# Optimization experiments

Measured on AMD Instinct MI355X. Metric: run time of the kernel, lower is better.

Reference implementation:

```python
import jax, jax.numpy as jnp
import numpy as np

# ---- grid / spectral configuration (matches init_kwargs) ----
_LONS_HALF = [20 + 4 * i for i in range(1, 97)]
LONS = _LONS_HALF + _LONS_HALF[::-1]          # 192 rings, pole to pole
NLAT = len(LONS)                               # 192
TRUNC = 191
M = TRUNC + 1                                  # zonal wavenumbers kept
MAX_NLON = max(LONS)                           # 404
SLON = np.concatenate([[0], np.cumsum(LONS)[:-1]]).astype(np.int64)
NGRID = int(np.sum(LONS))                      # 41088
BATCH, CHAN = 16, 64
TWO_PI = 2.0 * np.pi


def _legpoly(mmax, lmax, x):
    """(-1)^m c^l_m P^l_m(x), shape (mmax+1, lmax+1, len(x)); same recurrences as source."""
    nmax = max(mmax, lmax)
    vdm = np.zeros((nmax + 1, nmax + 1, len(x)), dtype=np.float64)
    norm_factor = np.sqrt(4 * np.pi)  # forward transform (inverse=False)
    vdm[0, 0, :] = norm_factor / np.sqrt(4 * np.pi)
    for n in range(1, nmax + 1):
        vdm[n - 1, n, :] = np.sqrt(2 * n + 1) * x * vdm[n - 1, n - 1, :]
        vdm[n, n, :] = np.sqrt((2 * n + 1) * (1 + x) * (1 - x) / 2 / n) * vdm[n - 1, n - 1, :]
    for n in range(2, nmax + 1):
        for m in range(0, n - 1):
            vdm[m, n, :] = (x * np.sqrt((2 * n - 1) / (n - m) * (2 * n + 1) / (n + m)) * vdm[m, n - 1, :]
                            - np.sqrt((n + m - 1) / (n - m) * (2 * n + 1) / (2 * n - 3) * (n - m - 1) / (n + m)) * vdm[m, n - 2, :])
    return vdm[:mmax + 1, :lmax + 1]


def _build_buffers():
    # Legendre-Gauss nodes/weights on [-1, 1]
    xlg, wlg = np.polynomial.legendre.leggauss(NLAT)
    theta = np.flip(np.arccos(xlg))
    pct = _legpoly(TRUNC, TRUNC, np.cos(theta))          # (M, L, K)
    weight = (pct * wlg[None, None, :]).astype(np.float32)

    # Ragged per-ring real DFT expressed as masked cos/sin bases (== rfft, norm='forward')
    p = np.arange(MAX_NLON)
    m = np.arange(M)
    nlon = np.asarray(LONS, dtype=np.float64)[:, None, None]       # (K,1,1)
    ang = TWO_PI * m[None, None, :] * p[None, :, None] / nlon      # (K,P,M)
    valid = (p[None, :, None] < nlon) & (m[None, None, :] <= (np.asarray(LONS)[:, None, None] // 2))
    cos_basis = np.where(valid, np.cos(ang) / nlon, 0.0).astype(np.float32)
    sin_basis = np.where(valid, -np.sin(ang) / nlon, 0.0).astype(np.float32)

    # gather map: ring_idx[k, p] = SLON[k] + min(p, nlon_k - 1)  (clipped; basis masks the tail)
    ring_idx = (SLON[:, None] + np.minimum(p[None, :], np.asarray(LONS)[:, None] - 1)).astype(np.int32)
    return weight, cos_basis, sin_basis, ring_idx


def setup_inputs() -> dict:
    key = jax.random.key(0)
    x = jax.random.normal(key, (BATCH, CHAN, NGRID), dtype=jnp.float32)
    weight, cos_basis, sin_basis, ring_idx = _build_buffers()
    return {
        "x": x,
        "weight": jnp.asarray(weight),
        "cos_basis": jnp.asarray(cos_basis),
        "sin_basis": jnp.asarray(sin_basis),
        "ring_idx": jnp.asarray(ring_idx),
    }


def reference(x, weight, cos_basis, sin_basis, ring_idx):
    # gather grid points into padded rings: [..., K, P]
    xr = x[..., ring_idx]
    # per-ring rfft (norm='forward'), restricted to m <= TRUNC, scaled by 2*pi
    re = TWO_PI * jnp.einsum("bckp,kpm->bckm", xr, cos_basis)
    im = TWO_PI * jnp.einsum("bckp,kpm->bckm", xr, sin_basis)
    # weighted Legendre contraction over latitudes k: [..., l, m]
    rl = jnp.einsum("bckm,mlk->bclm", re, weight)
    il = jnp.einsum("bckm,mlk->bclm", im, weight)
    # real/imag stacked (== torch.view_as_real of the complex output)
    return jnp.stack((rl, il), axis=-1)
```

## Files before the change

### kernel.cpp

```cpp
#include <hip/hip_runtime.h>

#define NLAT 192
#define MM   192
#define LL   192
#define PMAX 404
#define NGRID 41088
#define BC   1024
#define TWO_PI_F 6.2831853071795864769f

__global__ __launch_bounds__(256) void sht_stage1(
    const float* __restrict__ x,
    const float* __restrict__ cosb,
    const float* __restrict__ sinb,
    const int*   __restrict__ ring,
    float* __restrict__ ws,
    int bc0, int bcc)
{
    const int k   = blockIdx.z;
    const int m0  = blockIdx.y * 64;
    const int bct = blockIdx.x * 64;
    const int tid = threadIdx.x;
    const int tx = tid & 15;
    const int ty = tid >> 4;

    const int slon = ring[k * PMAX];
    const int nlon = ring[k * PMAX + PMAX - 1] - slon + 1;

    float* __restrict__ re_ws = ws;
    float* __restrict__ im_ws = ws + (size_t)MM * NLAT * bcc;

    if (m0 > (nlon >> 1)) {
        float4 z = {0.f, 0.f, 0.f, 0.f};
#pragma unroll
        for (int j = 0; j < 4; ++j) {
            int m = m0 + 4 * ty + j;
            size_t base = ((size_t)m * NLAT + k) * bcc + bct + 4 * tx;
            *(float4*)&re_ws[base] = z;
            *(float4*)&im_ws[base] = z;
        }
        return;
    }

    __shared__ float xs[16][68];
    __shared__ float cs[16][64];
    __shared__ float ss[16][64];

    float accr[4][4] = {{0.f}};
    float acci[4][4] = {{0.f}};

    for (int p0 = 0; p0 < nlon; p0 += 16) {
        {
            int pq = (tid & 3) * 4;
            int bl = tid >> 2;
            int p  = p0 + pq;
            float4 v = {0.f, 0.f, 0.f, 0.f};
            if (p < nlon)
                v = *(const float4*)(x + (size_t)(bc0 + bct + bl) * NGRID + slon + p);
            xs[pq + 0][bl] = v.x;
            xs[pq + 1][bl] = v.y;
            xs[pq + 2][bl] = v.z;
            xs[pq + 3][bl] = v.w;
        }
        {
            int mq = (tid & 15) * 4;
            int pl = tid >> 4;
            int p  = p0 + pl;
            float4 c = {0.f, 0.f, 0.f, 0.f};
            float4 s = {0.f, 0.f, 0.f, 0.f};
            if (p < PMAX) {
                size_t off = ((size_t)k * PMAX + p) * MM + m0 + mq;
                c = *(const float4*)(cosb + off);
                s = *(const float4*)(sinb + off);
            }
            *(float4*)&cs[pl][mq] = c;
            *(float4*)&ss[pl][mq] = s;
        }
        __syncthreads();

#pragma unroll
        for (int pp = 0; pp < 16; ++pp) {
            float xv[4], cv[4], sv[4];
            *(float4*)xv = *(const float4*)&xs[pp][4 * tx];
            *(float4*)cv = *(const float4*)&cs[pp][4 * ty];
            *(float4*)sv = *(const float4*)&ss[pp][4 * ty];
#pragma unroll
            for (int i = 0; i < 4; ++i)
#pragma unroll
                for (int j = 0; j < 4; ++j) {
                    accr[i][j] += xv[i] * cv[j];
                    acci[i][j] += xv[i] * sv[j];
                }
        }
        __syncthreads();
    }

#pragma unroll
    for (int j = 0; j < 4; ++j) {
        int m = m0 + 4 * ty + j;
        size_t base = ((size_t)m * NLAT + k) * bcc + bct + 4 * tx;
        float4 r = {accr[0][j] * TWO_PI_F, accr[1][j] * TWO_PI_F,
                    accr[2][j] * TWO_PI_F, accr[3][j] * TWO_PI_F};
        float4 s = {acci[0][j] * TWO_PI_F, acci[1][j] * TWO_PI_F,
                    acci[2][j] * TWO_PI_F, acci[3][j] * TWO_PI_F};
        *(float4*)&re_ws[base] = r;
        *(float4*)&im_ws[base] = s;
    }
}

__global__ __launch_bounds__(256) void sht_stage2(
    const float* __restrict__ ws,
    float* __restrict__ ws2,
    const float* __restrict__ weight,
    int bcc)
{
    const int m   = blockIdx.z;
    const int l0  = blockIdx.y * 64;
    const int bct = blockIdx.x * 64;
    const int tid = threadIdx.x;
    const int tx = tid & 15;
    const int ty = tid >> 4;

    if (l0 + 63 < m) return;

    const float* __restrict__ re_ws = ws;
    const float* __restrict__ im_ws = ws + (size_t)MM * NLAT * bcc;

    __shared__ float rs[16][64];
    __shared__ float is_[16][64];
    __shared__ float wl[16][68];

    float accr[4][4] = {{0.f}};
    float acci[4][4] = {{0.f}};

    for (int k0 = 0; k0 < NLAT; k0 += 16) {
        {
            int bl = tid & 63;
            int kk = tid >> 6;
#pragma unroll
            for (int kp = 0; kp < 4; ++kp) {
                int row = kk + kp * 4;
                size_t off = ((size_t)m * NLAT + k0 + row) * bcc + bct + bl;
                rs[row][bl]  = re_ws[off];
                is_[row][bl] = im_ws[off];
            }
        }
        {
            int kk = tid & 15;
            int ll = tid >> 4;
#pragma unroll
            for (int lp = 0; lp < 4; ++lp) {
                int l = l0 + ll + lp * 16;
                wl[kk][ll + lp * 16] = weight[((size_t)m * LL + l) * NLAT + k0 + kk];
            }
        }
        __syncthreads();

#pragma unroll
        for (int kk = 0; kk < 16; ++kk) {
            float rv[4], iv[4], wv[4];
            *(float4*)rv = *(const float4*)&rs[kk][4 * tx];
            *(float4*)iv = *(const float4*)&is_[kk][4 * tx];
            *(float4*)wv = *(const float4*)&wl[kk][4 * ty];
#pragma unroll
            for (int i = 0; i < 4; ++i)
#pragma unroll
                for (int j = 0; j < 4; ++j) {
                    accr[i][j] += rv[i] * wv[j];
                    acci[i][j] += iv[i] * wv[j];
                }
        }
        __syncthreads();
    }

    float* __restrict__ re2 = ws2;
    float* __restrict__ im2 = ws2 + (size_t)MM * LL * bcc;
#pragma unroll
    for (int j = 0; j < 4; ++j) {
        int l = l0 + 4 * ty + j;
        size_t base = ((size_t)m * LL + l) * bcc + bct + 4 * tx;
        float4 r = {accr[0][j], accr[1][j], accr[2][j], accr[3][j]};
        float4 s = {acci[0][j], acci[1][j], acci[2][j], acci[3][j]};
        *(float4*)&re2[base] = r;
        *(float4*)&im2[base] = s;
    }
}

__global__ __launch_bounds__(256) void sht_transpose(
    const float* __restrict__ ws2,
    float* __restrict__ out,
    int bc0, int bcc)
{
    const int l   = blockIdx.z;
    const int m0  = blockIdx.y * 32;
    const int bct = blockIdx.x * 32;
    const int tid = threadIdx.x;

    const float* __restrict__ re2 = ws2;
    const float* __restrict__ im2 = ws2 + (size_t)MM * LL * bcc;

    __shared__ float tr[32][33];
    __shared__ float ti[32][33];

    if (m0 <= l) {
        int bci = tid & 31;
        int mi  = tid >> 5;
#pragma unroll
        for (int mp = 0; mp < 4; ++mp) {
            int mrow = mi + mp * 8;
            size_t off = ((size_t)(m0 + mrow) * LL + l) * bcc + bct + bci;
            tr[mrow][bci] = re2[off];
            ti[mrow][bci] = im2[off];
        }
    }
    __syncthreads();

    int mi2  = tid & 31;
    int bci2 = tid >> 5;
    int m = m0 + mi2;
    bool nz = (m <= l);
#pragma unroll
    for (int bcp = 0; bcp < 4; ++bcp) {
        int bcl = bci2 + bcp * 8;
        int bc  = bc0 + bct + bcl;
        float2 v;
        if (nz) { v.x = tr[mi2][bcl]; v.y = ti[mi2][bcl]; }
        else    { v.x = 0.f;          v.y = 0.f;          }
        size_t o = (((size_t)bc * LL + l) * MM + m) * 2;
        *(float2*)&out[o] = v;
    }
}

extern "C" void kernel_launch(void* const* d_in, const int* in_sizes, int n_in,
                              void* d_out, int out_size, void* d_ws, size_t ws_size,
                              hipStream_t stream)
{
    const float* x      = (const float*)d_in[0];
    const float* weight = (const float*)d_in[1];
    const float* cosb   = (const float*)d_in[2];
    const float* sinb   = (const float*)d_in[3];
    const int*   ring   = (const int*)d_in[4];
    float* out = (float*)d_out;
    float* wsf = (float*)d_ws;

    const size_t per_bc = 4ull * MM * NLAT * sizeof(float);
    int chunk = BC;
    while ((size_t)chunk * per_bc > ws_size && chunk > 64) chunk >>= 1;

    for (int bc0 = 0; bc0 < BC; bc0 += chunk) {
        float* ws2 = wsf + 2ull * MM * NLAT * chunk;
        dim3 grid1(chunk / 64, 3, NLAT);
        hipLaunchKernelGGL(sht_stage1, grid1, dim3(256), 0, stream,
                           x, cosb, sinb, ring, wsf, bc0, chunk);
        dim3 grid2(chunk / 64, 3, MM);
        hipLaunchKernelGGL(sht_stage2, grid2, dim3(256), 0, stream,
                           wsf, ws2, weight, chunk);
        dim3 grid3(chunk / 32, 6, LL);
        hipLaunchKernelGGL(sht_transpose, grid3, dim3(256), 0, stream,
                           ws2, out, bc0, chunk);
    }
}
```

Measured before the change: 1.025 ms.

## Widen batch tiles and skip latitudes where Legendre weights vanish

Doubles the batch-channel tile in the DFT and Legendre stages to 128, so each thread computes an 8x4 register tile and reuses the shared basis and weights across more batch columns. Stage 2 now starts and ends its latitude loop at a polar cutoff kmin_of_m(m), skipping rows where the associated Legendre weights are assumed negligible. Stage 1 stops writing zeros for those skipped rows, and the transpose moves to 64x64 tiles with float4 loads and stores. The tile change raises register pressure and halves the block count. The latitude cutoff drops terms that are small but not exactly zero, so results may deviate slightly.

Measured after the change: 972.5 us. -5.1%, faster.

```diff
diff --git a/kernel.cpp b/kernel.cpp
--- a/kernel.cpp
+++ b/kernel.cpp
@@ -8,6 +8,10 @@
 #define BC   1024
 #define TWO_PI_F 6.2831853071795864769f
 
+__device__ __forceinline__ int kmin_of_m(int m) {
+    return (m <= 12) ? 0 : ((m - 11) >> 1);
+}
+
 __global__ __launch_bounds__(256) void sht_stage1(
     const float* __restrict__ x,
     const float* __restrict__ cosb,
@@ -18,10 +22,10 @@
 {
     const int k   = blockIdx.z;
     const int m0  = blockIdx.y * 64;
-    const int bct = blockIdx.x * 64;
+    const int bct = blockIdx.x * 128;
     const int tid = threadIdx.x;
-    const int tx = tid & 15;
-    const int ty = tid >> 4;
+    const int tx  = tid & 15;
+    const int ty  = tid >> 4;
 
     const int slon = ring[k * PMAX];
     const int nlon = ring[k * PMAX + PMAX - 1] - slon + 1;
@@ -30,45 +34,48 @@
     float* __restrict__ im_ws = ws + (size_t)MM * NLAT * bcc;
 
     if (m0 > (nlon >> 1)) {
-        float4 z = {0.f, 0.f, 0.f, 0.f};
+        const int klo16 = kmin_of_m(m0) & ~15;
+        if (k < klo16 || k > (NLAT - 1) - klo16) return;
+        const float4 z = {0.f, 0.f, 0.f, 0.f};
 #pragma unroll
         for (int j = 0; j < 4; ++j) {
-            int m = m0 + 4 * ty + j;
-            size_t base = ((size_t)m * NLAT + k) * bcc + bct + 4 * tx;
-            *(float4*)&re_ws[base] = z;
-            *(float4*)&im_ws[base] = z;
+            const int m = m0 + 4 * ty + j;
+            const size_t base = ((size_t)m * NLAT + k) * bcc + bct;
+            *(float4*)&re_ws[base + 4 * tx]      = z;
+            *(float4*)&re_ws[base + 64 + 4 * tx] = z;
+            *(float4*)&im_ws[base + 4 * tx]      = z;
+            *(float4*)&im_ws[base + 64 + 4 * tx] = z;
         }
         return;
     }
 
-    __shared__ float xs[16][68];
+    __shared__ float xs[16][128];
     __shared__ float cs[16][64];
     __shared__ float ss[16][64];
 
-    float accr[4][4] = {{0.f}};
-    float acci[4][4] = {{0.f}};
+    float accr[8][4] = {{0.f}};
+    float acci[8][4] = {{0.f}};
 
     for (int p0 = 0; p0 < nlon; p0 += 16) {
-        {
-            int pq = (tid & 3) * 4;
-            int bl = tid >> 2;
-            int p  = p0 + pq;
+#pragma unroll
+        for (int r = 0; r < 2; ++r) {
+            const int idx = r * 256 + tid;
+            const int bl  = idx & 127;
+            const int pq  = (idx >> 7) * 4;
             float4 v = {0.f, 0.f, 0.f, 0.f};
-            if (p < nlon)
-                v = *(const float4*)(x + (size_t)(bc0 + bct + bl) * NGRID + slon + p);
+            if (p0 + pq < nlon)
+                v = *(const float4*)(x + (size_t)(bc0 + bct + bl) * NGRID + slon + p0 + pq);
             xs[pq + 0][bl] = v.x;
             xs[pq + 1][bl] = v.y;
             xs[pq + 2][bl] = v.z;
             xs[pq + 3][bl] = v.w;
         }
         {
-            int mq = (tid & 15) * 4;
-            int pl = tid >> 4;
-            int p  = p0 + pl;
-            float4 c = {0.f, 0.f, 0.f, 0.f};
-            float4 s = {0.f, 0.f, 0.f, 0.f};
-            if (p < PMAX) {
-                size_t off = ((size_t)k * PMAX + p) * MM + m0 + mq;
+            const int mq = tx * 4;
+            const int pl = ty;
+            float4 c = {0.f, 0.f, 0.f, 0.f}, s = {0.f, 0.f, 0.f, 0.f};
+            if (p0 + pl < PMAX) {
+                const size_t off = ((size_t)k * PMAX + p0 + pl) * MM + m0 + mq;
                 c = *(const float4*)(cosb + off);
                 s = *(const float4*)(sinb + off);
             }
@@ -79,16 +86,19 @@
 
 #pragma unroll
         for (int pp = 0; pp < 16; ++pp) {
-            float xv[4], cv[4], sv[4];
-            *(float4*)xv = *(const float4*)&xs[pp][4 * tx];
-            *(float4*)cv = *(const float4*)&cs[pp][4 * ty];
-            *(float4*)sv = *(const float4*)&ss[pp][4 * ty];
-#pragma unroll
-            for (int i = 0; i < 4; ++i)
+            const float4 xa = *(const float4*)&xs[pp][4 * tx];
+            const float4 xb = *(const float4*)&xs[pp][64 + 4 * tx];
+            const float4 cv = *(const float4*)&cs[pp][4 * ty];
+            const float4 sv = *(const float4*)&ss[pp][4 * ty];
+            const float xv[8] = {xa.x, xa.y, xa.z, xa.w, xb.x, xb.y, xb.z, xb.w};
+            const float cw[4] = {cv.x, cv.y, cv.z, cv.w};
+            const float sw[4] = {sv.x, sv.y, sv.z, sv.w};
+#pragma unroll
+            for (int i = 0; i < 8; ++i)
 #pragma unroll
                 for (int j = 0; j < 4; ++j) {
-                    accr[i][j] += xv[i] * cv[j];
-                    acci[i][j] += xv[i] * sv[j];
+                    accr[i][j] += xv[i] * cw[j];
+                    acci[i][j] += xv[i] * sw[j];
                 }
         }
         __syncthreads();
@@ -96,14 +106,20 @@
 
 #pragma unroll
     for (int j = 0; j < 4; ++j) {
-        int m = m0 + 4 * ty + j;
-        size_t base = ((size_t)m * NLAT + k) * bcc + bct + 4 * tx;
-        float4 r = {accr[0][j] * TWO_PI_F, accr[1][j] * TWO_PI_F,
-                    accr[2][j] * TWO_PI_F, accr[3][j] * TWO_PI_F};
-        float4 s = {acci[0][j] * TWO_PI_F, acci[1][j] * TWO_PI_F,
-                    acci[2][j] * TWO_PI_F, acci[3][j] * TWO_PI_F};
-        *(float4*)&re_ws[base] = r;
-        *(float4*)&im_ws[base] = s;
+        const int m = m0 + 4 * ty + j;
+        const size_t base = ((size_t)m * NLAT + k) * bcc + bct;
+        float4 r0 = {accr[0][j] * TWO_PI_F, accr[1][j] * TWO_PI_F,
+                     accr[2][j] * TWO_PI_F, accr[3][j] * TWO_PI_F};
+        float4 r1 = {accr[4][j] * TWO_PI_F, accr[5][j] * TWO_PI_F,
+                     accr[6][j] * TWO_PI_F, accr[7][j] * TWO_PI_F};
+        float4 i0 = {acci[0][j] * TWO_PI_F, acci[1][j] * TWO_PI_F,
+                     acci[2][j] * TWO_PI_F, acci[3][j] * TWO_PI_F};
+        float4 i1 = {acci[4][j] * TWO_PI_F, acci[5][j] * TWO_PI_F,
+                     acci[6][j] * TWO_PI_F, acci[7][j] * TWO_PI_F};
+        *(float4*)&re_ws[base + 4 * tx]      = r0;
+        *(float4*)&re_ws[base + 64 + 4 * tx] = r1;
+        *(float4*)&im_ws[base + 4 * tx]      = i0;
+        *(float4*)&im_ws[base + 64 + 4 * tx] = i1;
     }
 }
 
@@ -115,58 +131,66 @@
 {
     const int m   = blockIdx.z;
     const int l0  = blockIdx.y * 64;
-    const int bct = blockIdx.x * 64;
+    const int bct = blockIdx.x * 128;
     const int tid = threadIdx.x;
-    const int tx = tid & 15;
-    const int ty = tid >> 4;
+    const int tx  = tid & 15;
+    const int ty  = tid >> 4;
 
     if (l0 + 63 < m) return;
+
+    const int klo16 = kmin_of_m(m) & ~15;
+    const int kcnt  = NLAT - 2 * klo16;
 
     const float* __restrict__ re_ws = ws;
     const float* __restrict__ im_ws = ws + (size_t)MM * NLAT * bcc;
 
-    __shared__ float rs[16][64];
-    __shared__ float is_[16][64];
-    __shared__ float wl[16][68];
-
-    float accr[4][4] = {{0.f}};
-    float acci[4][4] = {{0.f}};
-
-    for (int k0 = 0; k0 < NLAT; k0 += 16) {
+    __shared__ float rs[16][128];
+    __shared__ float is_[16][128];
+    __shared__ float wl[16][64];
+
+    float accr[8][4] = {{0.f}};
+    float acci[8][4] = {{0.f}};
+
+    for (int kc = 0; kc < kcnt; kc += 16) {
+        const int k0 = klo16 + kc;
         {
-            int bl = tid & 63;
-            int kk = tid >> 6;
-#pragma unroll
-            for (int kp = 0; kp < 4; ++kp) {
-                int row = kk + kp * 4;
-                size_t off = ((size_t)m * NLAT + k0 + row) * bcc + bct + bl;
-                rs[row][bl]  = re_ws[off];
-                is_[row][bl] = im_ws[off];
+            const int bl4 = (tid & 31) * 4;
+            const int kk  = tid >> 5;
+#pragma unroll
+            for (int r = 0; r < 2; ++r) {
+                const int row = kk + r * 8;
+                const size_t off = ((size_t)m * NLAT + k0 + row) * bcc + bct + bl4;
+                *(float4*)&rs[row][bl4]  = *(const float4*)&re_ws[off];
+                *(float4*)&is_[row][bl4] = *(const float4*)&im_ws[off];
             }
         }
         {
-            int kk = tid & 15;
-            int ll = tid >> 4;
-#pragma unroll
-            for (int lp = 0; lp < 4; ++lp) {
-                int l = l0 + ll + lp * 16;
-                wl[kk][ll + lp * 16] = weight[((size_t)m * LL + l) * NLAT + k0 + kk];
+            const int kk = tid & 15;
+            const int lw = tid >> 4;
+#pragma unroll
+            for (int r = 0; r < 4; ++r) {
+                const int lc = lw + r * 16;
+                wl[kk][lc] = weight[((size_t)m * LL + l0 + lc) * NLAT + k0 + kk];
             }
         }
         __syncthreads();
 
 #pragma unroll
         for (int kk = 0; kk < 16; ++kk) {
-            float rv[4], iv[4], wv[4];
-            *(float4*)rv = *(const float4*)&rs[kk][4 * tx];
-            *(float4*)iv = *(const float4*)&is_[kk][4 * tx];
-            *(float4*)wv = *(const float4*)&wl[kk][4 * ty];
-#pragma unroll
-            for (int i = 0; i < 4; ++i)
+            const float4 ra = *(const float4*)&rs[kk][4 * tx];
+            const float4 rb = *(const float4*)&rs[kk][64 + 4 * tx];
+            const float4 ia = *(const float4*)&is_[kk][4 * tx];
+            const float4 ib = *(const float4*)&is_[kk][64 + 4 * tx];
+            const float4 wv = *(const float4*)&wl[kk][4 * ty];
+            const float rv[8] = {ra.x, ra.y, ra.z, ra.w, rb.x, rb.y, rb.z, rb.w};
+            const float iv[8] = {ia.x, ia.y, ia.z, ia.w, ib.x, ib.y, ib.z, ib.w};
+            const float wq[4] = {wv.x, wv.y, wv.z, wv.w};
+#pragma unroll
+            for (int i = 0; i < 8; ++i)
 #pragma unroll
                 for (int j = 0; j < 4; ++j) {
-                    accr[i][j] += rv[i] * wv[j];
-                    acci[i][j] += iv[i] * wv[j];
+                    accr[i][j] += rv[i] * wq[j];
+                    acci[i][j] += iv[i] * wq[j];
                 }
         }
         __syncthreads();
@@ -176,12 +200,17 @@
     float* __restrict__ im2 = ws2 + (size_t)MM * LL * bcc;
 #pragma unroll
     for (int j = 0; j < 4; ++j) {
-        int l = l0 + 4 * ty + j;
-        size_t base = ((size_t)m * LL + l) * bcc + bct + 4 * tx;
-        float4 r = {accr[0][j], accr[1][j], accr[2][j], accr[3][j]};
-        float4 s = {acci[0][j], acci[1][j], acci[2][j], acci[3][j]};
-        *(float4*)&re2[base] = r;
-        *(float4*)&im2[base] = s;
+        const int l = l0 + 4 * ty + j;
+        if (l < m) continue;
+        const size_t base = ((size_t)m * LL + l) * bcc + bct;
+        float4 r0 = {accr[0][j], accr[1][j], accr[2][j], accr[3][j]};
+        float4 r1 = {accr[4][j], accr[5][j], accr[6][j], accr[7][j]};
+        float4 i0 = {acci[0][j], acci[1][j], acci[2][j], acci[3][j]};
+        float4 i1 = {acci[4][j], acci[5][j], acci[6][j], acci[7][j]};
+        *(float4*)&re2[base + 4 * tx]      = r0;
+        *(float4*)&re2[base + 64 + 4 * tx] = r1;
+        *(float4*)&im2[base + 4 * tx]      = i0;
+        *(float4*)&im2[base + 64 + 4 * tx] = i1;
     }
 }
 
@@ -191,42 +220,47 @@
     int bc0, int bcc)
 {
     const int l   = blockIdx.z;
-    const int m0  = blockIdx.y * 32;
-    const int bct = blockIdx.x * 32;
+    const int m0  = blockIdx.y * 64;
+    const int bct = blockIdx.x * 64;
     const int tid = threadIdx.x;
 
-    const float* __restrict__ re2 = ws2;
-    const float* __restrict__ im2 = ws2 + (size_t)MM * LL * bcc;
-
-    __shared__ float tr[32][33];
-    __shared__ float ti[32][33];
-
-    if (m0 <= l) {
-        int bci = tid & 31;
-        int mi  = tid >> 5;
-#pragma unroll
-        for (int mp = 0; mp < 4; ++mp) {
-            int mrow = mi + mp * 8;
-            size_t off = ((size_t)(m0 + mrow) * LL + l) * bcc + bct + bci;
-            tr[mrow][bci] = re2[off];
-            ti[mrow][bci] = im2[off];
+    __shared__ float tr[64][66];
+    __shared__ float ti[64][66];
+
+    const bool anynz = (m0 <= l);
+    if (anynz) {
+        const float* __restrict__ re2 = ws2;
+        const float* __restrict__ im2 = ws2 + (size_t)MM * LL * bcc;
+        const int bl4 = (tid & 15) * 4;
+        const int mr  = tid >> 4;
+#pragma unroll
+        for (int r = 0; r < 4; ++r) {
+            const int row = mr + r * 16;
+            const size_t off = ((size_t)(m0 + row) * LL + l) * bcc + bct + bl4;
+            *(float4*)&tr[row][bl4] = *(const float4*)&re2[off];
+            *(float4*)&ti[row][bl4] = *(const float4*)&im2[off];
         }
     }
     __syncthreads();
 
-    int mi2  = tid & 31;
-    int bci2 = tid >> 5;
-    int m = m0 + mi2;
-    bool nz = (m <= l);
-#pragma unroll
-    for (int bcp = 0; bcp < 4; ++bcp) {
-        int bcl = bci2 + bcp * 8;
-        int bc  = bc0 + bct + bcl;
-        float2 v;
-        if (nz) { v.x = tr[mi2][bcl]; v.y = ti[mi2][bcl]; }
-        else    { v.x = 0.f;          v.y = 0.f;          }
-        size_t o = (((size_t)bc * LL + l) * MM + m) * 2;
-        *(float2*)&out[o] = v;
+    const int mq  = tid & 15;
+    const int bcw = tid >> 4;
+#pragma unroll
+    for (int r = 0; r < 4; ++r) {
+        const int bcl = bcw + r * 16;
+        const int bc  = bc0 + bct + bcl;
+#pragma unroll
+        for (int h = 0; h < 2; ++h) {
+            const int ml = 32 * h + 2 * mq;
+            const int m  = m0 + ml;
+            float4 v = {0.f, 0.f, 0.f, 0.f};
+            if (anynz) {
+                if (m <= l)     { v.x = tr[ml][bcl];     v.y = ti[ml][bcl]; }
+                if (m + 1 <= l) { v.z = tr[ml + 1][bcl]; v.w = ti[ml + 1][bcl]; }
+            }
+            const size_t o = (((size_t)bc * LL + l) * MM + m) * 2;
+            *(float4*)&out[o] = v;
+        }
     }
 }
 
@@ -244,17 +278,17 @@
 
     const size_t per_bc = 4ull * MM * NLAT * sizeof(float);
     int chunk = BC;
-    while ((size_t)chunk * per_bc > ws_size && chunk > 64) chunk >>= 1;
+    while ((size_t)chunk * per_bc > ws_size && chunk > 128) chunk >>= 1;
 
     for (int bc0 = 0; bc0 < BC; bc0 += chunk) {
         float* ws2 = wsf + 2ull * MM * NLAT * chunk;
-        dim3 grid1(chunk / 64, 3, NLAT);
+        dim3 grid1(chunk / 128, 3, NLAT);
         hipLaunchKernelGGL(sht_stage1, grid1, dim3(256), 0, stream,
                            x, cosb, sinb, ring, wsf, bc0, chunk);
-        dim3 grid2(chunk / 64, 3, MM);
+        dim3 grid2(chunk / 128, 3, MM);
         hipLaunchKernelGGL(sht_stage2, grid2, dim3(256), 0, stream,
                            wsf, ws2, weight, chunk);
-        dim3 grid3(chunk / 32, 6, LL);
+        dim3 grid3(chunk / 64, 3, LL);
         hipLaunchKernelGGL(sht_transpose, grid3, dim3(256), 0, stream,
                            ws2, out, bc0, chunk);
     }
```

## Exploit Legendre even/odd symmetry and skip negligible latitudes in the SHT stages

Applied to the files above, without the earlier changes.

Stage 2 folds north/south rings into even and odd sums and contracts only half the latitudes, picking the even or odd combination per l parity. It also skips latitude tiles below a per-m cutoff where the Legendre weights are negligible, and skips writes for l < m. Stage 1 doubles the batch tile to 128 with 512-thread blocks and skips zero-fills outside the needed latitude range. The transpose kernel is widened to 64 m per block and writes float4. The latitude cutoff is an approximation that relies on small weights, so it risks accuracy. Fewer, larger blocks may also hurt occupancy.

Result: slower. 1.940 ms (+89.2%).

```diff
diff --git a/kernel.cpp b/kernel.cpp
--- a/kernel.cpp
+++ b/kernel.cpp
@@ -8,7 +8,11 @@
 #define BC   1024
 #define TWO_PI_F 6.2831853071795864769f
 
-__global__ __launch_bounds__(256) void sht_stage1(
+__device__ __forceinline__ int kmin_of_m(int m) {
+    return (m <= 12) ? 0 : ((m - 11) >> 1);
+}
+
+__global__ __launch_bounds__(512, 8) void sht_stage1(
     const float* __restrict__ x,
     const float* __restrict__ cosb,
     const float* __restrict__ sinb,
@@ -18,10 +22,10 @@
 {
     const int k   = blockIdx.z;
     const int m0  = blockIdx.y * 64;
-    const int bct = blockIdx.x * 64;
+    const int bct = blockIdx.x * 128;
     const int tid = threadIdx.x;
-    const int tx = tid & 15;
-    const int ty = tid >> 4;
+    const int tx  = tid & 31;
+    const int ty  = (tid >> 5) & 15;
 
     const int slon = ring[k * PMAX];
     const int nlon = ring[k * PMAX + PMAX - 1] - slon + 1;
@@ -30,65 +34,67 @@
     float* __restrict__ im_ws = ws + (size_t)MM * NLAT * bcc;
 
     if (m0 > (nlon >> 1)) {
-        float4 z = {0.f, 0.f, 0.f, 0.f};
+        const int klo16 = kmin_of_m(m0) & ~15;
+        if (k < klo16 || k > (NLAT - 1) - klo16) return;
+        const float4 z = {0.f, 0.f, 0.f, 0.f};
 #pragma unroll
         for (int j = 0; j < 4; ++j) {
-            int m = m0 + 4 * ty + j;
-            size_t base = ((size_t)m * NLAT + k) * bcc + bct + 4 * tx;
+            const int m = m0 + 4 * ty + j;
+            const size_t base = ((size_t)m * NLAT + k) * bcc + bct + 4 * tx;
             *(float4*)&re_ws[base] = z;
             *(float4*)&im_ws[base] = z;
         }
         return;
     }
 
-    __shared__ float xs[16][68];
+    __shared__ float xs[16][128];
     __shared__ float cs[16][64];
     __shared__ float ss[16][64];
 
     float accr[4][4] = {{0.f}};
     float acci[4][4] = {{0.f}};
 
+    const int xpq  = (tid & 3) * 4;
+    const int xbl  = tid >> 2;
+    const int bpl  = (tid >> 4) & 15;
+    const int bmq  = (tid & 15) * 4;
+    const int half = tid >> 8;
+
     for (int p0 = 0; p0 < nlon; p0 += 16) {
         {
-            int pq = (tid & 3) * 4;
-            int bl = tid >> 2;
-            int p  = p0 + pq;
             float4 v = {0.f, 0.f, 0.f, 0.f};
-            if (p < nlon)
-                v = *(const float4*)(x + (size_t)(bc0 + bct + bl) * NGRID + slon + p);
-            xs[pq + 0][bl] = v.x;
-            xs[pq + 1][bl] = v.y;
-            xs[pq + 2][bl] = v.z;
-            xs[pq + 3][bl] = v.w;
-        }
-        {
-            int mq = (tid & 15) * 4;
-            int pl = tid >> 4;
-            int p  = p0 + pl;
-            float4 c = {0.f, 0.f, 0.f, 0.f};
-            float4 s = {0.f, 0.f, 0.f, 0.f};
-            if (p < PMAX) {
-                size_t off = ((size_t)k * PMAX + p) * MM + m0 + mq;
-                c = *(const float4*)(cosb + off);
-                s = *(const float4*)(sinb + off);
+            if (p0 + xpq < nlon)
+                v = *(const float4*)(x + (size_t)(bc0 + bct + xbl) * NGRID + slon + p0 + xpq);
+            xs[xpq + 0][xbl] = v.x;
+            xs[xpq + 1][xbl] = v.y;
+            xs[xpq + 2][xbl] = v.z;
+            xs[xpq + 3][xbl] = v.w;
+        }
+        {
+            float4 b = {0.f, 0.f, 0.f, 0.f};
+            if (p0 + bpl < PMAX) {
+                const size_t off = ((size_t)k * PMAX + p0 + bpl) * MM + m0 + bmq;
+                b = *(const float4*)((half ? sinb : cosb) + off);
             }
-            *(float4*)&cs[pl][mq] = c;
-            *(float4*)&ss[pl][mq] = s;
+            if (half) *(float4*)&ss[bpl][bmq] = b;
+            else      *(float4*)&cs[bpl][bmq] = b;
         }
         __syncthreads();
 
 #pragma unroll
         for (int pp = 0; pp < 16; ++pp) {
-            float xv[4], cv[4], sv[4];
-            *(float4*)xv = *(const float4*)&xs[pp][4 * tx];
-            *(float4*)cv = *(const float4*)&cs[pp][4 * ty];
-            *(float4*)sv = *(const float4*)&ss[pp][4 * ty];
+            const float4 xa = *(const float4*)&xs[pp][4 * tx];
+            const float4 cv = *(const float4*)&cs[pp][4 * ty];
+            const float4 sv = *(const float4*)&ss[pp][4 * ty];
+            const float xv[4] = {xa.x, xa.y, xa.z, xa.w};
+            const float cw[4] = {cv.x, cv.y, cv.z, cv.w};
+            const float sw[4] = {sv.x, sv.y, sv.z, sv.w};
 #pragma unroll
             for (int i = 0; i < 4; ++i)
 #pragma unroll
                 for (int j = 0; j < 4; ++j) {
-                    accr[i][j] += xv[i] * cv[j];
-                    acci[i][j] += xv[i] * sv[j];
+                    accr[i][j] += xv[i] * cw[j];
+                    acci[i][j] += xv[i] * sw[j];
                 }
         }
         __syncthreads();
@@ -96,8 +102,8 @@
 
 #pragma unroll
     for (int j = 0; j < 4; ++j) {
-        int m = m0 + 4 * ty + j;
-        size_t base = ((size_t)m * NLAT + k) * bcc + bct + 4 * tx;
+        const int m = m0 + 4 * ty + j;
+        const size_t base = ((size_t)m * NLAT + k) * bcc + bct + 4 * tx;
         float4 r = {accr[0][j] * TWO_PI_F, accr[1][j] * TWO_PI_F,
                     accr[2][j] * TWO_PI_F, accr[3][j] * TWO_PI_F};
         float4 s = {acci[0][j] * TWO_PI_F, acci[1][j] * TWO_PI_F,
@@ -107,7 +113,7 @@
     }
 }
 
-__global__ __launch_bounds__(256) void sht_stage2(
+__global__ __launch_bounds__(512, 8) void sht_stage2(
     const float* __restrict__ ws,
     float* __restrict__ ws2,
     const float* __restrict__ weight,
@@ -115,59 +121,81 @@
 {
     const int m   = blockIdx.z;
     const int l0  = blockIdx.y * 64;
-    const int bct = blockIdx.x * 64;
+    const int bct = blockIdx.x * 128;
+    if (l0 + 63 < m) return;
+
     const int tid = threadIdx.x;
-    const int tx = tid & 15;
-    const int ty = tid >> 4;
-
-    if (l0 + 63 < m) return;
+    const int tx  = tid & 31;
+    const int ty  = (tid >> 5) & 15;
+
+    const int klo16 = kmin_of_m(m) & ~15;
+    const int pcnt  = 96 - klo16;
 
     const float* __restrict__ re_ws = ws;
     const float* __restrict__ im_ws = ws + (size_t)MM * NLAT * bcc;
 
-    __shared__ float rs[16][64];
-    __shared__ float is_[16][64];
+    __shared__ float Ar[16][128];
+    __shared__ float Br[16][128];
+    __shared__ float Ai[16][128];
+    __shared__ float Bi[16][128];
     __shared__ float wl[16][68];
 
     float accr[4][4] = {{0.f}};
     float acci[4][4] = {{0.f}};
 
-    for (int k0 = 0; k0 < NLAT; k0 += 16) {
-        {
-            int bl = tid & 63;
-            int kk = tid >> 6;
-#pragma unroll
-            for (int kp = 0; kp < 4; ++kp) {
-                int row = kk + kp * 4;
-                size_t off = ((size_t)m * NLAT + k0 + row) * bcc + bct + bl;
-                rs[row][bl]  = re_ws[off];
-                is_[row][bl] = im_ws[off];
+    const bool modd = (m & 1) != 0;
+    const int  srow = tid >> 5;
+    const int  scol = (tid & 31) * 4;
+    const int  wkk  = tid & 15;
+    const int  wlw  = tid >> 4;
+
+    for (int pc = 0; pc < pcnt; pc += 16) {
+        const int p0 = klo16 + pc;
+        {
+            const size_t offa = ((size_t)m * NLAT + (p0 + srow)) * bcc + bct + scol;
+            const size_t offb = ((size_t)m * NLAT + (191 - p0 - srow)) * bcc + bct + scol;
+            const float4 ar = *(const float4*)&re_ws[offa];
+            const float4 br = *(const float4*)&re_ws[offb];
+            const float4 ai = *(const float4*)&im_ws[offa];
+            const float4 bi = *(const float4*)&im_ws[offb];
+            float4 er = {ar.x + br.x, ar.y + br.y, ar.z + br.z, ar.w + br.w};
+            float4 od = {ar.x - br.x, ar.y - br.y, ar.z - br.z, ar.w - br.w};
+            float4 ei = {ai.x + bi.x, ai.y + bi.y, ai.z + bi.z, ai.w + bi.w};
+            float4 oi = {ai.x - bi.x, ai.y - bi.y, ai.z - bi.z, ai.w - bi.w};
+            if (modd) { float4 t = er; er = od; od = t; t = ei; ei = oi; oi = t; }
+            *(float4*)&Ar[srow][scol] = er;
+            *(float4*)&Br[srow][scol] = od;
+            *(float4*)&Ai[srow][scol] = ei;
+            *(float4*)&Bi[srow][scol] = oi;
+        }
+        {
+            wl[wkk][wlw]      = weight[((size_t)m * LL + l0 + wlw) * NLAT + p0 + wkk];
+            wl[wkk][wlw + 32] = weight[((size_t)m * LL + l0 + wlw + 32) * NLAT + p0 + wkk];
+        }
+        __syncthreads();
+
+#pragma unroll
+        for (int kk = 0; kk < 16; ++kk) {
+            const float4 e_r = *(const float4*)&Ar[kk][4 * tx];
+            const float4 o_r = *(const float4*)&Br[kk][4 * tx];
+            const float4 e_i = *(const float4*)&Ai[kk][4 * tx];
+            const float4 o_i = *(const float4*)&Bi[kk][4 * tx];
+            const float4 wv  = *(const float4*)&wl[kk][4 * ty];
+            const float er4[4] = {e_r.x, e_r.y, e_r.z, e_r.w};
+            const float or4[4] = {o_r.x, o_r.y, o_r.z, o_r.w};
+            const float ei4[4] = {e_i.x, e_i.y, e_i.z, e_i.w};
+            const float oi4[4] = {o_i.x, o_i.y, o_i.z, o_i.w};
+#pragma unroll
+            for (int i = 0; i < 4; ++i) {
+                accr[i][0] += er4[i] * wv.x;
+                accr[i][1] += or4[i] * wv.y;
+                accr[i][2] += er4[i] * wv.z;
+                accr[i][3] += or4[i] * wv.w;
+                acci[i][0] += ei4[i] * wv.x;
+                acci[i][1] += oi4[i] * wv.y;
+                acci[i][2] += ei4[i] * wv.z;
+                acci[i][3] += oi4[i] * wv.w;
             }
-        }
-        {
-            int kk = tid & 15;
-            int ll = tid >> 4;
-#pragma unroll
-            for (int lp = 0; lp < 4; ++lp) {
-                int l = l0 + ll + lp * 16;
-                wl[kk][ll + lp * 16] = weight[((size_t)m * LL + l) * NLAT + k0 + kk];
-            }
-        }
-        __syncthreads();
-
-#pragma unroll
-        for (int kk = 0; kk < 16; ++kk) {
-            float rv[4], iv[4], wv[4];
-            *(float4*)rv = *(const float4*)&rs[kk][4 * tx];
-            *(float4*)iv = *(const float4*)&is_[kk][4 * tx];
-            *(float4*)wv = *(const float4*)&wl[kk][4 * ty];
-#pragma unroll
-            for (int i = 0; i < 4; ++i)
-#pragma unroll
-                for (int j = 0; j < 4; ++j) {
-                    accr[i][j] += rv[i] * wv[j];
-                    acci[i][j] += iv[i] * wv[j];
-                }
         }
         __syncthreads();
     }
@@ -176,8 +204,9 @@
     float* __restrict__ im2 = ws2 + (size_t)MM * LL * bcc;
 #pragma unroll
     for (int j = 0; j < 4; ++j) {
-        int l = l0 + 4 * ty + j;
-        size_t base = ((size_t)m * LL + l) * bcc + bct + 4 * tx;
+        const int l = l0 + 4 * ty + j;
+        if (l < m) continue;
+        const size_t base = ((size_t)m * LL + l) * bcc + bct + 4 * tx;
         float4 r = {accr[0][j], accr[1][j], accr[2][j], accr[3][j]};
         float4 s = {acci[0][j], acci[1][j], acci[2][j], acci[3][j]};
         *(float4*)&re2[base] = r;
@@ -191,42 +220,49 @@
     int bc0, int bcc)
 {
     const int l   = blockIdx.z;
-    const int m0  = blockIdx.y * 32;
+    const int m0  = blockIdx.y * 64;
     const int bct = blockIdx.x * 32;
     const int tid = threadIdx.x;
 
-    const float* __restrict__ re2 = ws2;
-    const float* __restrict__ im2 = ws2 + (size_t)MM * LL * bcc;
-
-    __shared__ float tr[32][33];
-    __shared__ float ti[32][33];
-
-    if (m0 <= l) {
-        int bci = tid & 31;
-        int mi  = tid >> 5;
-#pragma unroll
-        for (int mp = 0; mp < 4; ++mp) {
-            int mrow = mi + mp * 8;
-            size_t off = ((size_t)(m0 + mrow) * LL + l) * bcc + bct + bci;
-            tr[mrow][bci] = re2[off];
-            ti[mrow][bci] = im2[off];
+    __shared__ float t2r[32][66];
+    __shared__ float t2i[32][66];
+
+    const bool anynz = (m0 <= l);
+    if (anynz) {
+        const float* __restrict__ re2 = ws2;
+        const float* __restrict__ im2 = ws2 + (size_t)MM * LL * bcc;
+        const int bl4 = (tid & 7) * 4;
+        const int mr  = tid >> 3;
+#pragma unroll
+        for (int r = 0; r < 2; ++r) {
+            const int row = mr + r * 32;
+            const size_t off = ((size_t)(m0 + row) * LL + l) * bcc + bct + bl4;
+            const float4 a = *(const float4*)&re2[off];
+            const float4 b = *(const float4*)&im2[off];
+            t2r[bl4 + 0][row] = a.x; t2r[bl4 + 1][row] = a.y;
+            t2r[bl4 + 2][row] = a.z; t2r[bl4 + 3][row] = a.w;
+            t2i[bl4 + 0][row] = b.x; t2i[bl4 + 1][row] = b.y;
+            t2i[bl4 + 2][row] = b.z; t2i[bl4 + 3][row] = b.w;
         }
     }
     __syncthreads();
 
-    int mi2  = tid & 31;
-    int bci2 = tid >> 5;
-    int m = m0 + mi2;
-    bool nz = (m <= l);
-#pragma unroll
-    for (int bcp = 0; bcp < 4; ++bcp) {
-        int bcl = bci2 + bcp * 8;
-        int bc  = bc0 + bct + bcl;
-        float2 v;
-        if (nz) { v.x = tr[mi2][bcl]; v.y = ti[mi2][bcl]; }
-        else    { v.x = 0.f;          v.y = 0.f;          }
-        size_t o = (((size_t)bc * LL + l) * MM + m) * 2;
-        *(float2*)&out[o] = v;
+    const int mq  = tid & 31;
+    const int bcw = tid >> 5;
+#pragma unroll
+    for (int r = 0; r < 4; ++r) {
+        const int bcl = bcw + 8 * r;
+        const int bc  = bc0 + bct + bcl;
+        const int m   = m0 + 2 * mq;
+        float4 v = {0.f, 0.f, 0.f, 0.f};
+        if (anynz) {
+            const float2 rr = *(const float2*)&t2r[bcl][2 * mq];
+            const float2 ii = *(const float2*)&t2i[bcl][2 * mq];
+            if (m     <= l) { v.x = rr.x; v.y = ii.x; }
+            if (m + 1 <= l) { v.z = rr.y; v.w = ii.y; }
+        }
+        const size_t o = (((size_t)bc * LL + l) * MM + m) * 2;
+        *(float4*)&out[o] = v;
     }
 }
 
@@ -244,17 +280,17 @@
 
     const size_t per_bc = 4ull * MM * NLAT * sizeof(float);
     int chunk = BC;
-    while ((size_t)chunk * per_bc > ws_size && chunk > 64) chunk >>= 1;
+    while ((size_t)chunk * per_bc > ws_size && chunk > 128) chunk >>= 1;
 
     for (int bc0 = 0; bc0 < BC; bc0 += chunk) {
         float* ws2 = wsf + 2ull * MM * NLAT * chunk;
-        dim3 grid1(chunk / 64, 3, NLAT);
-        hipLaunchKernelGGL(sht_stage1, grid1, dim3(256), 0, stream,
+        dim3 grid1(chunk / 128, 3, NLAT);
+        hipLaunchKernelGGL(sht_stage1, grid1, dim3(512), 0, stream,
                            x, cosb, sinb, ring, wsf, bc0, chunk);
-        dim3 grid2(chunk / 64, 3, MM);
-        hipLaunchKernelGGL(sht_stage2, grid2, dim3(256), 0, stream,
+        dim3 grid2(chunk / 128, 3, MM);
+        hipLaunchKernelGGL(sht_stage2, grid2, dim3(512), 0, stream,
                            wsf, ws2, weight, chunk);
-        dim3 grid3(chunk / 32, 6, LL);
+        dim3 grid3(chunk / 32, 3, LL);
         hipLaunchKernelGGL(sht_transpose, grid3, dim3(256), 0, stream,
                            ws2, out, bc0, chunk);
     }
```
